# Kernel tuning notes

Hardware: AMD Instinct MI355X
Metric: run time of the kernel (lower is better)

## Reference

```python
import jax, jax.numpy as jnp
import numpy as np

B, T, D_IN, H, D_OUT = 256, 512, 64, 256, 8


def setup_inputs() -> dict:
    key = jax.random.key(0)
    ks = jax.random.split(key, 6)
    s_ih = 1.0 / np.sqrt(H)
    inputs = jax.random.normal(ks[0], (B, T, D_IN), dtype=jnp.float32)
    h0 = jnp.zeros((B, H), dtype=jnp.float32)
    c0 = jnp.zeros((B, H), dtype=jnp.float32)
    # LSTM cell params, PyTorch gate order (i, f, g, o)
    W_ih = jax.random.uniform(ks[1], (4 * H, D_IN), minval=-s_ih, maxval=s_ih, dtype=jnp.float32)
    W_hh = jax.random.uniform(ks[2], (4 * H, H), minval=-s_ih, maxval=s_ih, dtype=jnp.float32)
    b = jax.random.uniform(ks[3], (4 * H,), minval=-s_ih, maxval=s_ih, dtype=jnp.float32)
    # output projection (xavier_uniform weight, zero bias)
    lim = np.sqrt(6.0 / (H + D_OUT))
    W_out = jax.random.uniform(ks[4], (D_OUT, H), minval=-lim, maxval=lim, dtype=jnp.float32)
    b_out = jnp.zeros((D_OUT,), dtype=jnp.float32)
    return {"inputs": inputs, "h0": h0, "c0": c0, "W_ih": W_ih, "W_hh": W_hh,
            "b": b, "W_out": W_out, "b_out": b_out}


def _lstm_last(inputs, h0, c0, W_ih, W_hh, b):
    # inputs: [B, T, D_in] -> scan over time, keep only final hidden state
    xs = jnp.swapaxes(inputs, 0, 1)  # [T, B, D_in]

    def step(carry, x_t):
        h, c = carry
        gates = x_t @ W_ih.T + h @ W_hh.T + b  # [B, 4H]
        i, f, g, o = jnp.split(gates, 4, axis=-1)
        c_new = jax.nn.sigmoid(f) * c + jax.nn.sigmoid(i) * jnp.tanh(g)
        h_new = jax.nn.sigmoid(o) * jnp.tanh(c_new)
        return (h_new, c_new), None

    (h, c), _ = jax.lax.scan(step, (h0, c0), xs)
    return h, c


def reference(inputs, h0, c0, W_ih, W_hh, b, W_out, b_out):
    h, c = _lstm_last(inputs, h0, c0, W_ih, W_hh, b)
    rnn_outputs = h  # last-timestep output (dropout_prob=0 -> identity)
    logits = rnn_outputs @ W_out.T + b_out
    return (rnn_outputs, logits, h, c)
```

## Files before the change

### kernel.cpp

```cpp
#include <hip/hip_runtime.h>

#define T_ 512
#define B_ 256
#define H_ 256
#define DIN_ 64

typedef __attribute__((ext_vector_type(8))) short short8;
typedef __attribute__((ext_vector_type(4))) float f32x4;
typedef __attribute__((ext_vector_type(4))) unsigned int u32x4;

__device__ __forceinline__ unsigned short f2bf(float f) {
  unsigned u = __float_as_uint(f);
  u += 0x7FFFu + ((u >> 16) & 1u);
  return (unsigned short)(u >> 16);
}
__device__ __forceinline__ float bf2f(unsigned short s) {
  return __uint_as_float(((unsigned)s) << 16);
}
__device__ __forceinline__ float sigm(float x) { return 1.0f / (1.0f + __expf(-x)); }
__device__ __forceinline__ float tanh_(float x) {
  float xx = fminf(fmaxf(x, -30.0f), 30.0f);
  float e = __expf(2.0f * xx);
  return (e - 1.0f) / (e + 1.0f);
}

__device__ __forceinline__ void load16_sc1(const unsigned* p, u32x4& a,
                                           u32x4& b, u32x4& c, u32x4& d) {
  asm volatile(
      "global_load_dwordx4 %0, %4, off sc1\n\t"
      "global_load_dwordx4 %1, %4, off offset:16 sc1\n\t"
      "global_load_dwordx4 %2, %4, off offset:32 sc1\n\t"
      "global_load_dwordx4 %3, %4, off offset:48 sc1\n\t"
      "s_waitcnt vmcnt(0)"
      : "=v"(a), "=v"(b), "=v"(c), "=v"(d)
      : "v"(p) : "memory");
}

__device__ __forceinline__ bool tags_ok(u32x4 a, u32x4 b, u32x4 c, u32x4 d,
                                        unsigned w) {
  unsigned m = (a.x >> 16) ^ w; m |= (a.y >> 16) ^ w;
  m |= (a.z >> 16) ^ w;         m |= (a.w >> 16) ^ w;
  m |= (b.x >> 16) ^ w;         m |= (b.y >> 16) ^ w;
  m |= (b.z >> 16) ^ w;         m |= (b.w >> 16) ^ w;
  m |= (c.x >> 16) ^ w;         m |= (c.y >> 16) ^ w;
  m |= (c.z >> 16) ^ w;         m |= (c.w >> 16) ^ w;
  m |= (d.x >> 16) ^ w;         m |= (d.y >> 16) ^ w;
  m |= (d.z >> 16) ^ w;         m |= (d.w >> 16) ^ w;
  return m == 0;
}

__global__ __launch_bounds__(256) void lstm_kern(
    const float* __restrict__ xin, const float* __restrict__ h0f,
    const float* __restrict__ c0f, const float* __restrict__ Wih,
    const float* __restrict__ Whh, const float* __restrict__ bias,
    const float* __restrict__ Wout, const float* __restrict__ bout,
    float* __restrict__ out, unsigned* hbuf32)
{
  const int tid = threadIdx.x;
  const int gb  = blockIdx.x >> 4;
  const int gc  = blockIdx.x & 15;
  const int wv  = tid >> 6;
  const int ln  = tid & 63;
  const int colB = ln & 15;
  const int krow = ln >> 4;

  __shared__ unsigned short h_s[16 * 264];
  __shared__ unsigned short x_s[16 * 72];
  __shared__ float gbuf[4 * 16 * 17];

  const int j = wv * H_ + gc * 16 + colB;
  short8 bh[8], bx[2];
  #pragma unroll
  for (int kc = 0; kc < 8; ++kc) {
    const float* p = Whh + j * H_ + kc * 32 + krow * 8;
    short8 f;
    #pragma unroll
    for (int i = 0; i < 8; ++i) f[i] = (short)f2bf(p[i]);
    bh[kc] = f;
  }
  #pragma unroll
  for (int kc = 0; kc < 2; ++kc) {
    const float* p = Wih + j * DIN_ + kc * 32 + krow * 8;
    short8 f;
    #pragma unroll
    for (int i = 0; i < 8; ++i) f[i] = (short)f2bf(p[i]);
    bx[kc] = f;
  }
  const float bval = bias[j];

  const int er = tid >> 4, ec = tid & 15;
  const int grow = gb * 16 + er;
  float c_val = c0f[grow * H_ + gc * 16 + ec];
  float h_val = 0.0f;

  const int xr = tid >> 4, xd = (tid & 15) * 4;
  const float* xrow = xin + (gb * 16 + xr) * (T_ * DIN_) + xd;
  float4 xcur = *(const float4*)(xrow);

  const int hr = tid >> 4;
  const int hcb = (tid & 15) * 16;
  const unsigned* ldp_base = hbuf32 + gb * 4096 + hr * 256 + hcb;
  unsigned* stp_base = hbuf32 + gb * 4096 + er * 256 + gc * 16 + ec;

  for (int s = 1; s <= T_; ++s) {
    {
      unsigned short* q = &x_s[xr * 72 + xd];
      q[0] = f2bf(xcur.x); q[1] = f2bf(xcur.y);
      q[2] = f2bf(xcur.z); q[3] = f2bf(xcur.w);
      const int tn = (s < T_) ? s : (T_ - 1);
      xcur = *(const float4*)(xrow + tn * DIN_);
    }

    if (s == 1) {
      #pragma unroll
      for (int it = 0; it < 4; ++it) {
        int e4 = tid + it * 256;
        int r = e4 >> 6, c4 = e4 & 63;
        const float4* p = (const float4*)(h0f + (gb * 16 + r) * H_) + c4;
        float4 v = *p;
        unsigned short* q = &h_s[r * 264 + c4 * 4];
        q[0] = f2bf(v.x); q[1] = f2bf(v.y); q[2] = f2bf(v.z); q[3] = f2bf(v.w);
      }
    } else {
      const unsigned want = (unsigned)(s - 1);
      const unsigned* ldp = ldp_base + (((s - 1) & 1) << 16);
      u32x4 va, vb, vc, vd;
      int tries = 0;
      do {
        load16_sc1(ldp, va, vb, vc, vd);
        if (tags_ok(va, vb, vc, vd, want)) break;
      } while (++tries < (1 << 18));
      unsigned* q32 = (unsigned*)&h_s[hr * 264 + hcb];
      q32[0] = (va.x & 0xFFFFu) | (va.y << 16);
      q32[1] = (va.z & 0xFFFFu) | (va.w << 16);
      q32[2] = (vb.x & 0xFFFFu) | (vb.y << 16);
      q32[3] = (vb.z & 0xFFFFu) | (vb.w << 16);
      q32[4] = (vc.x & 0xFFFFu) | (vc.y << 16);
      q32[5] = (vc.z & 0xFFFFu) | (vc.w << 16);
      q32[6] = (vd.x & 0xFFFFu) | (vd.y << 16);
      q32[7] = (vd.z & 0xFFFFu) | (vd.w << 16);
    }
    __syncthreads();

    f32x4 acc = {0.f, 0.f, 0.f, 0.f};
    #pragma unroll
    for (int kc = 0; kc < 2; ++kc) {
      short8 a = *(const short8*)&x_s[colB * 72 + kc * 32 + krow * 8];
      acc = __builtin_amdgcn_mfma_f32_16x16x32_bf16(a, bx[kc], acc, 0, 0, 0);
    }
    #pragma unroll
    for (int kc = 0; kc < 8; ++kc) {
      short8 a = *(const short8*)&h_s[colB * 264 + kc * 32 + krow * 8];
      acc = __builtin_amdgcn_mfma_f32_16x16x32_bf16(a, bh[kc], acc, 0, 0, 0);
    }
    #pragma unroll
    for (int i = 0; i < 4; ++i)
      gbuf[wv * 272 + (krow * 4 + i) * 17 + colB] = acc[i] + bval;
    __syncthreads();

    float gi = gbuf[0 * 272 + er * 17 + ec];
    float gf = gbuf[1 * 272 + er * 17 + ec];
    float gg = gbuf[2 * 272 + er * 17 + ec];
    float go = gbuf[3 * 272 + er * 17 + ec];
    c_val = sigm(gf) * c_val + sigm(gi) * tanh_(gg);
    h_val = sigm(go) * tanh_(c_val);

    unsigned pk = ((unsigned)s << 16) | (unsigned)f2bf(h_val);
    __hip_atomic_store(stp_base + ((s & 1) << 16), pk,
                       __ATOMIC_RELAXED, __HIP_MEMORY_SCOPE_AGENT);
  }

  const int gj = gc * 16 + ec;
  out[grow * H_ + gj] = h_val;
  out[67584 + grow * H_ + gj] = h_val;
  out[133120 + grow * H_ + gj] = c_val;

  if (gc == 0) {
    const unsigned want = (unsigned)T_;
    const unsigned* ldp = ldp_base + ((T_ & 1) << 16);
    u32x4 va, vb, vc, vd;
    int tries = 0;
    do {
      load16_sc1(ldp, va, vb, vc, vd);
      if (tags_ok(va, vb, vc, vd, want)) break;
    } while (++tries < (1 << 18));
    unsigned* q32 = (unsigned*)&h_s[hr * 264 + hcb];
    q32[0] = (va.x & 0xFFFFu) | (va.y << 16);
    q32[1] = (va.z & 0xFFFFu) | (va.w << 16);
    q32[2] = (vb.x & 0xFFFFu) | (vb.y << 16);
    q32[3] = (vb.z & 0xFFFFu) | (vb.w << 16);
    q32[4] = (vc.x & 0xFFFFu) | (vc.y << 16);
    q32[5] = (vc.z & 0xFFFFu) | (vc.w << 16);
    q32[6] = (vd.x & 0xFFFFu) | (vd.y << 16);
    q32[7] = (vd.z & 0xFFFFu) | (vd.w << 16);
    __syncthreads();
    if (tid < 128) {
      int r = tid >> 3, o = tid & 7;
      float a = bout[o];
      for (int k = 0; k < H_; ++k)
        a = fmaf(bf2f(h_s[r * 264 + k]), Wout[o * H_ + k], a);
      out[65536 + (gb * 16 + r) * 8 + o] = a;
    }
  }
}

extern "C" void kernel_launch(void* const* d_in, const int* in_sizes, int n_in,
                              void* d_out, int out_size, void* d_ws, size_t ws_size,
                              hipStream_t stream) {
  const float* xin  = (const float*)d_in[0];
  const float* h0f  = (const float*)d_in[1];
  const float* c0f  = (const float*)d_in[2];
  const float* Wih  = (const float*)d_in[3];
  const float* Whh  = (const float*)d_in[4];
  const float* bias = (const float*)d_in[5];
  const float* Wout = (const float*)d_in[6];
  const float* bout = (const float*)d_in[7];
  float* out = (float*)d_out;

  unsigned* hbuf32 = (unsigned*)d_ws;

  void* args[] = {&xin, &h0f, &c0f, &Wih, &Whh, &bias, &Wout, &bout,
                  &out, &hbuf32};
  hipLaunchCooperativeKernel((void*)lstm_kern, dim3(256), dim3(256),
                             args, 0, stream);
}
```

Baseline: 1.151 ms.

## Use 64 blocks of 1024 threads, each covering 64 hidden columns

Changes the work split from 256 blocks of 256 threads (16 hidden columns each) to 64 blocks of 1024 threads, each computing 64 hidden columns for 16 batch rows. Each block now owns a larger share of the recurrent state, so fewer blocks poll the cross-block buffer each step. Every thread polls a single 16-byte chunk instead of 64 bytes, which spreads the spin loads across more lanes. The trade-off is fewer CUs in use and a larger per-block barrier with 16 waves, and each wave still holds its slice of the weights in registers.

Result: slower. 1.314 ms (+14.2%).

```diff
diff --git a/kernel.cpp b/kernel.cpp
--- a/kernel.cpp
+++ b/kernel.cpp
@@ -24,32 +24,21 @@
   return (e - 1.0f) / (e + 1.0f);
 }
 
-__device__ __forceinline__ void load16_sc1(const unsigned* p, u32x4& a,
-                                           u32x4& b, u32x4& c, u32x4& d) {
+__device__ __forceinline__ void load4_sc1(const unsigned* p, u32x4& a) {
   asm volatile(
-      "global_load_dwordx4 %0, %4, off sc1\n\t"
-      "global_load_dwordx4 %1, %4, off offset:16 sc1\n\t"
-      "global_load_dwordx4 %2, %4, off offset:32 sc1\n\t"
-      "global_load_dwordx4 %3, %4, off offset:48 sc1\n\t"
+      "global_load_dwordx4 %0, %1, off sc1\n\t"
       "s_waitcnt vmcnt(0)"
-      : "=v"(a), "=v"(b), "=v"(c), "=v"(d)
+      : "=&v"(a)
       : "v"(p) : "memory");
 }
 
-__device__ __forceinline__ bool tags_ok(u32x4 a, u32x4 b, u32x4 c, u32x4 d,
-                                        unsigned w) {
+__device__ __forceinline__ bool tags_ok1(u32x4 a, unsigned w) {
   unsigned m = (a.x >> 16) ^ w; m |= (a.y >> 16) ^ w;
   m |= (a.z >> 16) ^ w;         m |= (a.w >> 16) ^ w;
-  m |= (b.x >> 16) ^ w;         m |= (b.y >> 16) ^ w;
-  m |= (b.z >> 16) ^ w;         m |= (b.w >> 16) ^ w;
-  m |= (c.x >> 16) ^ w;         m |= (c.y >> 16) ^ w;
-  m |= (c.z >> 16) ^ w;         m |= (c.w >> 16) ^ w;
-  m |= (d.x >> 16) ^ w;         m |= (d.y >> 16) ^ w;
-  m |= (d.z >> 16) ^ w;         m |= (d.w >> 16) ^ w;
   return m == 0;
 }
 
-__global__ __launch_bounds__(256) void lstm_kern(
+__global__ __launch_bounds__(1024) void lstm_kern(
     const float* __restrict__ xin, const float* __restrict__ h0f,
     const float* __restrict__ c0f, const float* __restrict__ Wih,
     const float* __restrict__ Whh, const float* __restrict__ bias,
@@ -57,18 +46,20 @@
     float* __restrict__ out, unsigned* hbuf32)
 {
   const int tid = threadIdx.x;
-  const int gb  = blockIdx.x >> 4;
-  const int gc  = blockIdx.x & 15;
+  const int gb  = blockIdx.x & 15;
+  const int gq  = blockIdx.x >> 4;
   const int wv  = tid >> 6;
   const int ln  = tid & 63;
+  const int g   = wv & 3;
+  const int hb  = wv >> 2;
   const int colB = ln & 15;
   const int krow = ln >> 4;
 
   __shared__ unsigned short h_s[16 * 264];
   __shared__ unsigned short x_s[16 * 72];
-  __shared__ float gbuf[4 * 16 * 17];
-
-  const int j = wv * H_ + gc * 16 + colB;
+  __shared__ float gbuf[4 * 16 * 68];
+
+  const int j = g * H_ + gq * 64 + hb * 16 + colB;
   short8 bh[8], bx[2];
   #pragma unroll
   for (int kc = 0; kc < 8; ++kc) {
@@ -88,22 +79,24 @@
   }
   const float bval = bias[j];
 
-  const int er = tid >> 4, ec = tid & 15;
+  const int er = tid >> 6, ec = tid & 63;
   const int grow = gb * 16 + er;
-  float c_val = c0f[grow * H_ + gc * 16 + ec];
+  const int gcol = gq * 64 + ec;
+  float c_val = c0f[grow * H_ + gcol];
   float h_val = 0.0f;
 
   const int xr = tid >> 4, xd = (tid & 15) * 4;
-  const float* xrow = xin + (gb * 16 + xr) * (T_ * DIN_) + xd;
-  float4 xcur = *(const float4*)(xrow);
-
-  const int hr = tid >> 4;
-  const int hcb = (tid & 15) * 16;
+  const float* xrow = xin + (gb * 16 + (xr & 15)) * (T_ * DIN_) + xd;
+  float4 xcur{};
+  if (tid < 256) xcur = *(const float4*)(xrow);
+
+  const int hr  = tid >> 6;
+  const int hcb = (tid & 63) * 4;
   const unsigned* ldp_base = hbuf32 + gb * 4096 + hr * 256 + hcb;
-  unsigned* stp_base = hbuf32 + gb * 4096 + er * 256 + gc * 16 + ec;
+  unsigned* stp_base = hbuf32 + gb * 4096 + er * 256 + gcol;
 
   for (int s = 1; s <= T_; ++s) {
-    {
+    if (tid < 256) {
       unsigned short* q = &x_s[xr * 72 + xd];
       q[0] = f2bf(xcur.x); q[1] = f2bf(xcur.y);
       q[2] = f2bf(xcur.z); q[3] = f2bf(xcur.w);
@@ -112,33 +105,22 @@
     }
 
     if (s == 1) {
-      #pragma unroll
-      for (int it = 0; it < 4; ++it) {
-        int e4 = tid + it * 256;
-        int r = e4 >> 6, c4 = e4 & 63;
-        const float4* p = (const float4*)(h0f + (gb * 16 + r) * H_) + c4;
-        float4 v = *p;
-        unsigned short* q = &h_s[r * 264 + c4 * 4];
-        q[0] = f2bf(v.x); q[1] = f2bf(v.y); q[2] = f2bf(v.z); q[3] = f2bf(v.w);
-      }
+      int r = tid >> 6, c4 = tid & 63;
+      float4 v = ((const float4*)(h0f + (gb * 16 + r) * H_))[c4];
+      unsigned short* q = &h_s[r * 264 + c4 * 4];
+      q[0] = f2bf(v.x); q[1] = f2bf(v.y); q[2] = f2bf(v.z); q[3] = f2bf(v.w);
     } else {
       const unsigned want = (unsigned)(s - 1);
       const unsigned* ldp = ldp_base + (((s - 1) & 1) << 16);
-      u32x4 va, vb, vc, vd;
+      u32x4 va;
       int tries = 0;
       do {
-        load16_sc1(ldp, va, vb, vc, vd);
-        if (tags_ok(va, vb, vc, vd, want)) break;
+        load4_sc1(ldp, va);
+        if (tags_ok1(va, want)) break;
       } while (++tries < (1 << 18));
       unsigned* q32 = (unsigned*)&h_s[hr * 264 + hcb];
       q32[0] = (va.x & 0xFFFFu) | (va.y << 16);
       q32[1] = (va.z & 0xFFFFu) | (va.w << 16);
-      q32[2] = (vb.x & 0xFFFFu) | (vb.y << 16);
-      q32[3] = (vb.z & 0xFFFFu) | (vb.w << 16);
-      q32[4] = (vc.x & 0xFFFFu) | (vc.y << 16);
-      q32[5] = (vc.z & 0xFFFFu) | (vc.w << 16);
-      q32[6] = (vd.x & 0xFFFFu) | (vd.y << 16);
-      q32[7] = (vd.z & 0xFFFFu) | (vd.w << 16);
     }
     __syncthreads();
 
@@ -155,13 +137,13 @@
     }
     #pragma unroll
     for (int i = 0; i < 4; ++i)
-      gbuf[wv * 272 + (krow * 4 + i) * 17 + colB] = acc[i] + bval;
+      gbuf[g * 1088 + (krow * 4 + i) * 68 + hb * 16 + colB] = acc[i] + bval;
     __syncthreads();
 
-    float gi = gbuf[0 * 272 + er * 17 + ec];
-    float gf = gbuf[1 * 272 + er * 17 + ec];
-    float gg = gbuf[2 * 272 + er * 17 + ec];
-    float go = gbuf[3 * 272 + er * 17 + ec];
+    float gi = gbuf[0 * 1088 + er * 68 + ec];
+    float gf = gbuf[1 * 1088 + er * 68 + ec];
+    float gg = gbuf[2 * 1088 + er * 68 + ec];
+    float go = gbuf[3 * 1088 + er * 68 + ec];
     c_val = sigm(gf) * c_val + sigm(gi) * tanh_(gg);
     h_val = sigm(go) * tanh_(c_val);
 
@@ -170,29 +152,22 @@
                        __ATOMIC_RELAXED, __HIP_MEMORY_SCOPE_AGENT);
   }
 
-  const int gj = gc * 16 + ec;
-  out[grow * H_ + gj] = h_val;
-  out[67584 + grow * H_ + gj] = h_val;
-  out[133120 + grow * H_ + gj] = c_val;
-
-  if (gc == 0) {
+  out[grow * H_ + gcol] = h_val;
+  out[67584 + grow * H_ + gcol] = h_val;
+  out[133120 + grow * H_ + gcol] = c_val;
+
+  if (gq == 0) {
     const unsigned want = (unsigned)T_;
     const unsigned* ldp = ldp_base + ((T_ & 1) << 16);
-    u32x4 va, vb, vc, vd;
+    u32x4 va;
     int tries = 0;
     do {
-      load16_sc1(ldp, va, vb, vc, vd);
-      if (tags_ok(va, vb, vc, vd, want)) break;
+      load4_sc1(ldp, va);
+      if (tags_ok1(va, want)) break;
     } while (++tries < (1 << 18));
     unsigned* q32 = (unsigned*)&h_s[hr * 264 + hcb];
     q32[0] = (va.x & 0xFFFFu) | (va.y << 16);
     q32[1] = (va.z & 0xFFFFu) | (va.w << 16);
-    q32[2] = (vb.x & 0xFFFFu) | (vb.y << 16);
-    q32[3] = (vb.z & 0xFFFFu) | (vb.w << 16);
-    q32[4] = (vc.x & 0xFFFFu) | (vc.y << 16);
-    q32[5] = (vc.z & 0xFFFFu) | (vc.w << 16);
-    q32[6] = (vd.x & 0xFFFFu) | (vd.y << 16);
-    q32[7] = (vd.z & 0xFFFFu) | (vd.w << 16);
     __syncthreads();
     if (tid < 128) {
       int r = tid >> 3, o = tid & 7;
@@ -221,6 +196,6 @@
 
   void* args[] = {&xin, &h0f, &c0f, &Wih, &Whh, &bias, &Wout, &bout,
                   &out, &hbuf32};
-  hipLaunchCooperativeKernel((void*)lstm_kern, dim3(256), dim3(256),
+  hipLaunchCooperativeKernel((void*)lstm_kern, dim3(64), dim3(1024),
                              args, 0, stream);
 }
```
